# Kernel optimization log

Hardware: AMD Instinct MI355X
Metric: run time of the kernel (lower is better)

Reference implementation:

```python
import jax, jax.numpy as jnp
import numpy as np
import math

B, N, D = 16, 1024, 1024

def setup_inputs() -> dict:
    key = jax.random.key(0)
    k1, k2, k3, k4 = jax.random.split(key, 4)
    x = jax.random.normal(k1, (B, N, D), dtype=jnp.float32)
    # Keras 'random_normal' initializer defaults to stddev=0.05
    w_keys = jax.random.normal(k2, (N, N), dtype=jnp.float32) * 0.05
    w_queries = jax.random.normal(k3, (N, N), dtype=jnp.float32) * 0.05
    w_values = jax.random.normal(k4, (N, N), dtype=jnp.float32) * 0.05
    return {"x": x, "w_keys": w_keys, "w_queries": w_queries, "w_values": w_values}

def reference(x, w_keys, w_queries, w_values):
    # x: (B, N, D); weights: (N, N); fact = sqrt(N) per build(input_shape[1])
    fact = math.sqrt(x.shape[1])
    ip = jnp.swapaxes(x, 1, 2)              # (B, D, N)
    vk = ip @ w_keys                         # (B, D, N)
    vq = ip @ w_queries                      # (B, D, N)
    vv = ip @ w_values                       # (B, D, N)
    kq = jnp.einsum('bdn,ben->bde', vk, vq) / fact   # (B, D, D)
    sm = jax.nn.softmax(kq, axis=-1)         # softmax over last axis
    # tf: sm @ transpose(pm(vv)) == sm @ vv  since pm then transpose_b cancel
    out = jnp.einsum('bde,ben->bdn', sm, vv) # (B, D, N)
    return jnp.swapaxes(out, 1, 2)           # (B, N, D)
```

## Files before the change

### kernel.cpp

```cpp
#include <hip/hip_runtime.h>
#include <stdint.h>


typedef __bf16 bf16x8_t __attribute__((ext_vector_type(8)));
typedef float  f32x4_t  __attribute__((ext_vector_type(4)));

typedef __attribute__((address_space(3))) uint32_t as3_u32;
typedef __attribute__((address_space(1))) uint32_t as1_u32;

__device__ __forceinline__ void async_copy16(const void* g, const void* l) {
  __builtin_amdgcn_global_load_lds((const as1_u32*)(uintptr_t)g,
                                   (as3_u32*)(uint32_t)(uintptr_t)l,
                                   16, 0, 0);
}

__device__ __forceinline__ uint16_t f2bf(float f) {
  uint32_t x = __float_as_uint(f);
  return (uint16_t)((x + 0x7fffu + ((x >> 16) & 1u)) >> 16);
}
__device__ __forceinline__ float bf2f(uint16_t b) {
  return __uint_as_float(((uint32_t)b) << 16);
}

template <int EPI>
__device__ __forceinline__ void gemm_body(
    const uint16_t* __restrict__ A, const uint16_t* __restrict__ B,
    void* __restrict__ Cv, size_t sA, size_t sB, size_t sC,
    float alpha, float* __restrict__ Sp, int lid, char* smem)
{
  char* As = smem;
  char* Bs = smem + 32768;

  const int xcd  = lid & 7;
  const int slot = lid >> 3;
  const int z    = (xcd << 1) | (slot >> 5);
  const int t32  = slot & 31;
  const int bm0  = (t32 >> 3) << 8;
  const int bn0  = (t32 & 7) << 7;

  A += (size_t)z * sA + ((size_t)bm0 << 10);
  B += (size_t)z * sB + ((size_t)bn0 << 10);

  const int t    = threadIdx.x;
  const int lane = t & 63;
  const int w    = t >> 6;
  const int q    = lane >> 4;
  const int r16  = lane & 15;
  const int wm   = (w >> 1) << 6;
  const int wn   = (w & 1) << 6;

  const int g0  = t >> 3;
  const int cp  = t & 7;
  const int ce  = (cp ^ (g0 & 7)) << 3;
  const int so  = (g0 << 7) + (cp << 4);
  const uint16_t* Ag = A + ((size_t)g0 << 10) + ce;
  const uint16_t* Bg = B + ((size_t)g0 << 10) + ce;

  f32x4_t acc[4][4];
#pragma unroll
  for (int i = 0; i < 4; i++)
#pragma unroll
    for (int j = 0; j < 4; j++) acc[i][j] = (f32x4_t){0.f, 0.f, 0.f, 0.f};

  for (int k0 = 0; k0 < 1024; k0 += 64) {
#pragma unroll
    for (int s = 0; s < 4; ++s)
      async_copy16(Ag + (((size_t)s << 6) << 10) + k0, As + so + (s << 13));
#pragma unroll
    for (int s = 0; s < 2; ++s)
      async_copy16(Bg + (((size_t)s << 6) << 10) + k0, Bs + so + (s << 13));
    __syncthreads();

#pragma unroll
    for (int kk = 0; kk < 2; ++kk) {
      bf16x8_t af[4], bfr[4];
#pragma unroll
      for (int mi = 0; mi < 4; ++mi) {
        const int m = wm + (mi << 4) + r16;
        const int c = (kk << 2) + q;
        af[mi] = *(const bf16x8_t*)(As + (m << 7) + ((c ^ (m & 7)) << 4));
      }
#pragma unroll
      for (int ni = 0; ni < 4; ++ni) {
        const int n = wn + (ni << 4) + r16;
        const int c = (kk << 2) + q;
        bfr[ni] = *(const bf16x8_t*)(Bs + (n << 7) + ((c ^ (n & 7)) << 4));
      }
      __builtin_amdgcn_s_setprio(1);
#pragma unroll
      for (int mi = 0; mi < 4; ++mi)
#pragma unroll
        for (int ni = 0; ni < 4; ++ni)
          acc[mi][ni] = __builtin_amdgcn_mfma_f32_16x16x32_bf16(
              af[mi], bfr[ni], acc[mi][ni], 0, 0, 0);
      __builtin_amdgcn_s_setprio(0);
    }
    __syncthreads();
  }

  if constexpr (EPI == 3) {
    float inv[4];
#pragma unroll
    for (int ni = 0; ni < 4; ++ni) {
      const int c = bn0 + wn + (ni << 4) + r16;
      float S = 0.f;
#pragma unroll
      for (int p = 0; p < 16; ++p)
        S += Sp[((size_t)p << 14) + ((size_t)z << 10) + c];
      inv[ni] = 1.0f / S;
    }
    float* C = (float*)Cv + (size_t)z * sC;
#pragma unroll
    for (int mi = 0; mi < 4; ++mi)
#pragma unroll
      for (int ni = 0; ni < 4; ++ni)
#pragma unroll
        for (int r = 0; r < 4; ++r) {
          const int row = bm0 + wm + (mi << 4) + (q << 2) + r;
          const int col = bn0 + wn + (ni << 4) + r16;
          C[((size_t)row << 10) + col] = acc[mi][ni][r] * alpha * inv[ni];
        }
  } else {
    float* reg = (float*)smem + (size_t)w * 1056;
    uint16_t* C = (uint16_t*)Cv + (size_t)z * sC;
    float* SpW = Sp + ((size_t)(((bn0 >> 7) << 1) + (w & 1)) << 14)
                    + ((size_t)z << 10);
#pragma unroll
    for (int mi = 0; mi < 4; ++mi) {
      if constexpr (EPI == 2) {
        float ev[4][4];
#pragma unroll
        for (int ni = 0; ni < 4; ++ni)
#pragma unroll
          for (int r = 0; r < 4; ++r) {
            ev[ni][r] = __expf(acc[mi][ni][r] * alpha);
            reg[((q << 2) + r) * 66 + (ni << 4) + r16] = ev[ni][r];
          }
#pragma unroll
        for (int r = 0; r < 4; ++r) {
          float s = ev[0][r] + ev[1][r] + ev[2][r] + ev[3][r];
          s += __shfl_xor(s, 1, 16);
          s += __shfl_xor(s, 2, 16);
          s += __shfl_xor(s, 4, 16);
          s += __shfl_xor(s, 8, 16);
          if (r16 == 0)
            SpW[bm0 + wm + (mi << 4) + (q << 2) + r] = s;
        }
      } else {
#pragma unroll
        for (int ni = 0; ni < 4; ++ni)
#pragma unroll
          for (int r = 0; r < 4; ++r)
            reg[((q << 2) + r) * 66 + (ni << 4) + r16] = acc[mi][ni][r] * alpha;
      }
#pragma unroll
      for (int it = 0; it < 8; ++it) {
        const int rr = (it << 1) + (lane >> 5);
        const int cc = (lane & 31) << 1;
        const float2 v = *(const float2*)(reg + rr * 66 + cc);
        const uint32_t p = (uint32_t)f2bf(v.x) | ((uint32_t)f2bf(v.y) << 16);
        const int row = bm0 + wm + (mi << 4) + rr;
        const int col = bn0 + wn + cc;
        *(uint32_t*)(C + ((size_t)row << 10) + col) = p;
      }
    }
  }
}

template <int EPI>
__global__ __launch_bounds__(512, 4)
void gemm_bt256x128(const uint16_t* __restrict__ A,
                    const uint16_t* __restrict__ B,
                    void* __restrict__ Cv, size_t sA, size_t sB, size_t sC,
                    float alpha, float* __restrict__ Sp)
{
  __shared__ __align__(16) char smem[49152];
  gemm_body<EPI>(A, B, Cv, sA, sB, sC, alpha, Sp, blockIdx.x, smem);
}

__global__ __launch_bounds__(512, 4)
void gemm_pair(const uint16_t* __restrict__ A0, const uint16_t* __restrict__ B0,
               void* __restrict__ C0, size_t sA0, size_t sB0, size_t sC0,
               const uint16_t* __restrict__ A1, const uint16_t* __restrict__ B1,
               void* __restrict__ C1, size_t sA1, size_t sB1, size_t sC1)
{
  __shared__ __align__(16) char smem[49152];
  const int lid = blockIdx.x;
  if (lid < 512)
    gemm_body<0>(A0, B0, C0, sA0, sB0, sC0, 1.0f, nullptr, lid, smem);
  else
    gemm_body<0>(A1, B1, C1, sA1, sB1, sC1, 1.0f, nullptr, lid - 512, smem);
}

__global__ __launch_bounds__(256)
void transpose_splitk(const float* __restrict__ x, uint16_t* __restrict__ xT,
                      const uint16_t* __restrict__ Wqc,
                      const uint16_t* __restrict__ Wkc,
                      float* __restrict__ W2p)
{
  __shared__ __align__(16) char smem[32768];
  const int bx = blockIdx.x;
  const int t  = threadIdx.x;

  if (bx < 4096) {
    float (*tile)[65] = (float(*)[65])smem;
    const int z  = bx >> 8;
    const int r0 = ((bx >> 4) & 15) << 6;
    const int c0 = (bx & 15) << 6;
    const float* src = x + ((size_t)z << 20);
    uint16_t* dst = xT + ((size_t)z << 20);
    const int row  = t >> 4;
    const int col4 = (t & 15) << 2;
#pragma unroll
    for (int i = 0; i < 4; ++i) {
      const float4 v = *(const float4*)(
          src + (size_t)(r0 + row + (i << 4)) * 1024 + c0 + col4);
      float* tp = &tile[row + (i << 4)][col4];
      tp[0] = v.x; tp[1] = v.y; tp[2] = v.z; tp[3] = v.w;
    }
    __syncthreads();
#pragma unroll
    for (int p = 0; p < 2; ++p) {
      const int idx = (p << 8) + t;
      const int c  = idx >> 3;
      const int s8 = (idx & 7) << 3;
      uint32_t u0 = (uint32_t)f2bf(tile[s8 + 0][c]) |
                    ((uint32_t)f2bf(tile[s8 + 1][c]) << 16);
      uint32_t u1 = (uint32_t)f2bf(tile[s8 + 2][c]) |
                    ((uint32_t)f2bf(tile[s8 + 3][c]) << 16);
      uint32_t u2 = (uint32_t)f2bf(tile[s8 + 4][c]) |
                    ((uint32_t)f2bf(tile[s8 + 5][c]) << 16);
      uint32_t u3 = (uint32_t)f2bf(tile[s8 + 6][c]) |
                    ((uint32_t)f2bf(tile[s8 + 7][c]) << 16);
      uint4 pk; pk.x = u0; pk.y = u1; pk.z = u2; pk.w = u3;
      *(uint4*)(dst + (size_t)(c0 + c) * 1024 + r0 + s8) = pk;
    }
    return;
  }

  char* As = smem;
  char* Bs = smem + 16384;
  const int lid   = bx - 4096;
  const int slice = lid >> 6;
  const int tile4 = lid & 63;
  const int bm0   = (tile4 >> 3) << 7;
  const int bn0   = (tile4 & 7) << 7;
  const int koff  = slice << 8;

  const int lane = t & 63;
  const int w    = t >> 6;
  const int q    = lane >> 4;
  const int r16  = lane & 15;
  const int wm   = (w >> 1) << 6;
  const int wn   = (w & 1) << 6;

  f32x4_t acc[4][4];
#pragma unroll
  for (int i = 0; i < 4; i++)
#pragma unroll
    for (int j = 0; j < 4; j++) acc[i][j] = (f32x4_t){0.f, 0.f, 0.f, 0.f};

  for (int k0 = koff; k0 < koff + 256; k0 += 64) {
#pragma unroll
    for (int i = 0; i < 4; i++) {
      const int o  = (i << 12) + (t << 4);
      const int m  = o >> 7;
      const int cp = (o >> 4) & 7;
      const int c  = cp ^ (m & 7);
      async_copy16(Wqc + (size_t)(bm0 + m) * 1024 + (size_t)(k0 + (c << 3)),
                   As + o);
      async_copy16(Wkc + (size_t)(bn0 + m) * 1024 + (size_t)(k0 + (c << 3)),
                   Bs + o);
    }
    __syncthreads();
#pragma unroll
    for (int kk = 0; kk < 2; kk++) {
      bf16x8_t af[4], bfr[4];
#pragma unroll
      for (int mi = 0; mi < 4; mi++) {
        const int m = wm + (mi << 4) + r16;
        const int c = (kk << 2) + q;
        af[mi] = *(const bf16x8_t*)(As + (m << 7) + ((c ^ (m & 7)) << 4));
      }
#pragma unroll
      for (int ni = 0; ni < 4; ni++) {
        const int n = wn + (ni << 4) + r16;
        const int c = (kk << 2) + q;
        bfr[ni] = *(const bf16x8_t*)(Bs + (n << 7) + ((c ^ (n & 7)) << 4));
      }
#pragma unroll
      for (int mi = 0; mi < 4; mi++)
#pragma unroll
        for (int ni = 0; ni < 4; ni++)
          acc[mi][ni] = __builtin_amdgcn_mfma_f32_16x16x32_bf16(
              af[mi], bfr[ni], acc[mi][ni], 0, 0, 0);
    }
    __syncthreads();
  }

  float* C = W2p + (size_t)slice * (1024u * 1024u);
#pragma unroll
  for (int mi = 0; mi < 4; mi++)
#pragma unroll
    for (int ni = 0; ni < 4; ni++)
#pragma unroll
      for (int r = 0; r < 4; r++) {
        const int row = bm0 + wm + (mi << 4) + (q << 2) + r;
        const int col = bn0 + wn + (ni << 4) + r16;
        C[((size_t)row << 10) + col] = acc[mi][ni][r];
      }
}

__global__ __launch_bounds__(256)
void reduce_w2t(const float* __restrict__ P, uint16_t* __restrict__ W)
{
  const size_t i4 = (((size_t)blockIdx.x << 8) + threadIdx.x) << 2;
  const float4 a = *(const float4*)(P + i4);
  const float4 b = *(const float4*)(P + (1u << 20) + i4);
  const float4 c = *(const float4*)(P + (2u << 20) + i4);
  const float4 d = *(const float4*)(P + (3u << 20) + i4);
  ushort4 r;
  r.x = f2bf(a.x + b.x + c.x + d.x);
  r.y = f2bf(a.y + b.y + c.y + d.y);
  r.z = f2bf(a.z + b.z + c.z + d.z);
  r.w = f2bf(a.w + b.w + c.w + d.w);
  *(ushort4*)(W + i4) = r;
}

__global__ __launch_bounds__(256)
void prep_w(const float* __restrict__ w0, const float* __restrict__ w1,
            const float* __restrict__ w2, uint16_t* __restrict__ o0,
            uint16_t* __restrict__ o1, uint16_t* __restrict__ o2)
{
  __shared__ float tile[32][33];
  const int z = blockIdx.z;
  const int c0 = blockIdx.x << 5;
  const int r0 = blockIdx.y << 5;
  const int t = threadIdx.x;
  if (z < 2) {
    const float* src = z ? w1 : w0;
    uint16_t* dst = z ? o1 : o0;
    const int row = t >> 3;
    const int c4  = (t & 7) << 2;
    const float4 v =
        *(const float4*)(src + (size_t)(r0 + row) * 1024 + c0 + c4);
    ushort4 u;
    u.x = f2bf(v.x); u.y = f2bf(v.y); u.z = f2bf(v.z); u.w = f2bf(v.w);
    *(ushort4*)(dst + (size_t)(r0 + row) * 1024 + c0 + c4) = u;
  } else {
    const int tx = t & 31, ty = t >> 5;
#pragma unroll
    for (int i = 0; i < 32; i += 8)
      tile[ty + i][tx] = w2[(size_t)(r0 + ty + i) * 1024 + (c0 + tx)];
    __syncthreads();
#pragma unroll
    for (int i = 0; i < 32; i += 8)
      o2[(size_t)(c0 + ty + i) * 1024 + (r0 + tx)] = f2bf(tile[tx][ty + i]);
  }
}

extern "C" void kernel_launch(void* const* d_in, const int* in_sizes, int n_in,
                              void* d_out, int out_size, void* d_ws, size_t ws_size,
                              hipStream_t stream)
{
  const float* x  = (const float*)d_in[0];
  const float* wk = (const float*)d_in[1];
  const float* wq = (const float*)d_in[2];
  const float* wv = (const float*)d_in[3];
  float* out = (float*)d_out;

  constexpr int N = 1024;
  constexpr size_t DN = (size_t)N * N;

  char* ws = (char*)d_ws;
  uint16_t* xT   = (uint16_t*)(ws);
  uint16_t* Wkc  = (uint16_t*)(ws + (32ull << 20));
  uint16_t* Wqc  = (uint16_t*)(ws + (34ull << 20));
  uint16_t* Wtv  = (uint16_t*)(ws + (36ull << 20));
  uint16_t* W2Tc = (uint16_t*)(ws + (38ull << 20));
  float*    W2p  = (float*)   (ws + (40ull << 20));
  uint16_t* tmp  = (uint16_t*)(ws + (56ull << 20));
  uint16_t* vvT  = (uint16_t*)(ws + (88ull << 20));
  uint16_t* P    = (uint16_t*)(ws + (120ull << 20));
  float*    Spart= (float*)   (ws + (152ull << 20));

  prep_w<<<dim3(N / 32, N / 32, 3), 256, 0, stream>>>(wk, wq, wv, Wkc, Wqc, Wtv);
  transpose_splitk<<<4352, 256, 0, stream>>>(x, xT, Wqc, Wkc, W2p);
  reduce_w2t<<<1024, 256, 0, stream>>>(W2p, W2Tc);
  gemm_pair<<<1024, 512, 0, stream>>>(xT, W2Tc, tmp, DN, 0, DN,
                                      Wtv, xT, vvT, 0, DN, DN);
  gemm_bt256x128<2><<<512, 512, 0, stream>>>(tmp, xT, P, DN, DN, DN, 0.03125f, Spart);
  gemm_bt256x128<3><<<512, 512, 0, stream>>>(vvT, P, out, DN, DN, DN, 1.0f, Spart);
}
```

Baseline: 278.6 us.

## Fuse weight prep, Wq·Wkᵀ product and x transpose into one launch

Three launches (weight conversion, transpose plus split-K weight GEMM, partial-sum reduction) become one kernel. The Wq·Wkᵀ product is now computed by 64 blocks over the full K, converting fp32 to bf16 on the fly while staging into LDS. This removes the fp32 partial buffer, the reduction pass and two launch gaps. The tradeoff is that only 64 blocks each run a 1024-deep K loop with synchronous loads, which may lengthen the critical path while the other blocks do the transpose.

```diff
diff --git a/kernel.cpp b/kernel.cpp
--- a/kernel.cpp
+++ b/kernel.cpp
@@ -193,20 +193,102 @@
 }
 
 __global__ __launch_bounds__(256)
-void transpose_splitk(const float* __restrict__ x, uint16_t* __restrict__ xT,
-                      const uint16_t* __restrict__ Wqc,
-                      const uint16_t* __restrict__ Wkc,
-                      float* __restrict__ W2p)
+void prep_all(const float* __restrict__ x, uint16_t* __restrict__ xT,
+              const float* __restrict__ wq, const float* __restrict__ wk,
+              const float* __restrict__ wv, uint16_t* __restrict__ W2Tc,
+              uint16_t* __restrict__ Wtv)
 {
   __shared__ __align__(16) char smem[32768];
   const int bx = blockIdx.x;
   const int t  = threadIdx.x;
 
-  if (bx < 4096) {
+  if (bx < 64) {
+    char* As = smem;
+    char* Bs = smem + 16384;
+    const int bm0 = (bx >> 3) << 7;
+    const int bn0 = (bx & 7) << 7;
+    const int lane = t & 63;
+    const int w4 = t >> 6;
+    const int q = lane >> 4;
+    const int r16 = lane & 15;
+    const int wm = (w4 >> 1) << 6;
+    const int wn = (w4 & 1) << 6;
+    const int g0 = t >> 1;
+    const int kh = (t & 1) << 5;
+    const float* srcA = wq + (size_t)(bm0 + g0) * 1024 + kh;
+    const float* srcB = wk + (size_t)(bn0 + g0) * 1024 + kh;
+
+    f32x4_t acc[4][4];
+#pragma unroll
+    for (int i = 0; i < 4; i++)
+#pragma unroll
+      for (int j = 0; j < 4; j++) acc[i][j] = (f32x4_t){0.f, 0.f, 0.f, 0.f};
+
+    for (int k0 = 0; k0 < 1024; k0 += 64) {
+#pragma unroll
+      for (int j = 0; j < 4; ++j) {
+        const int c  = ((t & 1) << 2) + j;
+        const int cp = c ^ (g0 & 7);
+        const float4 a0 = *(const float4*)(srcA + k0 + (j << 3));
+        const float4 a1 = *(const float4*)(srcA + k0 + (j << 3) + 4);
+        const float4 b0 = *(const float4*)(srcB + k0 + (j << 3));
+        const float4 b1 = *(const float4*)(srcB + k0 + (j << 3) + 4);
+        uint4 pa, pb;
+        pa.x = (uint32_t)f2bf(a0.x) | ((uint32_t)f2bf(a0.y) << 16);
+        pa.y = (uint32_t)f2bf(a0.z) | ((uint32_t)f2bf(a0.w) << 16);
+        pa.z = (uint32_t)f2bf(a1.x) | ((uint32_t)f2bf(a1.y) << 16);
+        pa.w = (uint32_t)f2bf(a1.z) | ((uint32_t)f2bf(a1.w) << 16);
+        pb.x = (uint32_t)f2bf(b0.x) | ((uint32_t)f2bf(b0.y) << 16);
+        pb.y = (uint32_t)f2bf(b0.z) | ((uint32_t)f2bf(b0.w) << 16);
+        pb.z = (uint32_t)f2bf(b1.x) | ((uint32_t)f2bf(b1.y) << 16);
+        pb.w = (uint32_t)f2bf(b1.z) | ((uint32_t)f2bf(b1.w) << 16);
+        *(uint4*)(As + (g0 << 7) + (cp << 4)) = pa;
+        *(uint4*)(Bs + (g0 << 7) + (cp << 4)) = pb;
+      }
+      __syncthreads();
+#pragma unroll
+      for (int kk = 0; kk < 2; kk++) {
+        bf16x8_t af[4], bfr[4];
+#pragma unroll
+        for (int mi = 0; mi < 4; mi++) {
+          const int m = wm + (mi << 4) + r16;
+          const int c = (kk << 2) + q;
+          af[mi] = *(const bf16x8_t*)(As + (m << 7) + ((c ^ (m & 7)) << 4));
+        }
+#pragma unroll
+        for (int ni = 0; ni < 4; ni++) {
+          const int n = wn + (ni << 4) + r16;
+          const int c = (kk << 2) + q;
+          bfr[ni] = *(const bf16x8_t*)(Bs + (n << 7) + ((c ^ (n & 7)) << 4));
+        }
+#pragma unroll
+        for (int mi = 0; mi < 4; mi++)
+#pragma unroll
+          for (int ni = 0; ni < 4; ni++)
+            acc[mi][ni] = __builtin_amdgcn_mfma_f32_16x16x32_bf16(
+                af[mi], bfr[ni], acc[mi][ni], 0, 0, 0);
+      }
+      __syncthreads();
+    }
+#pragma unroll
+    for (int mi = 0; mi < 4; mi++)
+#pragma unroll
+      for (int ni = 0; ni < 4; ni++)
+#pragma unroll
+        for (int r = 0; r < 4; r++) {
+          const int row = bm0 + wm + (mi << 4) + (q << 2) + r;
+          const int col = bn0 + wn + (ni << 4) + r16;
+          W2Tc[((size_t)row << 10) + col] = f2bf(acc[mi][ni][r]);
+        }
+    return;
+  }
+
+  if (bx < 4160) {
     float (*tile)[65] = (float(*)[65])smem;
-    const int z  = bx >> 8;
-    const int r0 = ((bx >> 4) & 15) << 6;
-    const int c0 = (bx & 15) << 6;
+    const int bxx = bx - 64;
+    const int z  = bxx >> 8;
+    const int r0 = ((bxx >> 4) & 15) << 6;
+    const int c0 = (bxx & 15) << 6;
     const float* src = x + ((size_t)z << 20);
     uint16_t* dst = xT + ((size_t)z << 20);
     const int row  = t >> 4;
@@ -238,124 +320,19 @@
     return;
   }
 
-  char* As = smem;
-  char* Bs = smem + 16384;
-  const int lid   = bx - 4096;
-  const int slice = lid >> 6;
-  const int tile4 = lid & 63;
-  const int bm0   = (tile4 >> 3) << 7;
-  const int bn0   = (tile4 & 7) << 7;
-  const int koff  = slice << 8;
-
-  const int lane = t & 63;
-  const int w    = t >> 6;
-  const int q    = lane >> 4;
-  const int r16  = lane & 15;
-  const int wm   = (w >> 1) << 6;
-  const int wn   = (w & 1) << 6;
-
-  f32x4_t acc[4][4];
-#pragma unroll
-  for (int i = 0; i < 4; i++)
-#pragma unroll
-    for (int j = 0; j < 4; j++) acc[i][j] = (f32x4_t){0.f, 0.f, 0.f, 0.f};
-
-  for (int k0 = koff; k0 < koff + 256; k0 += 64) {
-#pragma unroll
-    for (int i = 0; i < 4; i++) {
-      const int o  = (i << 12) + (t << 4);
-      const int m  = o >> 7;
-      const int cp = (o >> 4) & 7;
-      const int c  = cp ^ (m & 7);
-      async_copy16(Wqc + (size_t)(bm0 + m) * 1024 + (size_t)(k0 + (c << 3)),
-                   As + o);
-      async_copy16(Wkc + (size_t)(bn0 + m) * 1024 + (size_t)(k0 + (c << 3)),
-                   Bs + o);
-    }
+  {
+    float (*tile)[33] = (float(*)[33])smem;
+    const int bxw = bx - 4160;
+    const int r0 = (bxw >> 5) << 5;
+    const int c0 = (bxw & 31) << 5;
+    const int tx = t & 31, ty = t >> 5;
+#pragma unroll
+    for (int i = 0; i < 32; i += 8)
+      tile[ty + i][tx] = wv[(size_t)(r0 + ty + i) * 1024 + (c0 + tx)];
     __syncthreads();
 #pragma unroll
-    for (int kk = 0; kk < 2; kk++) {
-      bf16x8_t af[4], bfr[4];
-#pragma unroll
-      for (int mi = 0; mi < 4; mi++) {
-        const int m = wm + (mi << 4) + r16;
-        const int c = (kk << 2) + q;
-        af[mi] = *(const bf16x8_t*)(As + (m << 7) + ((c ^ (m & 7)) << 4));
-      }
-#pragma unroll
-      for (int ni = 0; ni < 4; ni++) {
-        const int n = wn + (ni << 4) + r16;
-        const int c = (kk << 2) + q;
-        bfr[ni] = *(const bf16x8_t*)(Bs + (n << 7) + ((c ^ (n & 7)) << 4));
-      }
-#pragma unroll
-      for (int mi = 0; mi < 4; mi++)
-#pragma unroll
-        for (int ni = 0; ni < 4; ni++)
-          acc[mi][ni] = __builtin_amdgcn_mfma_f32_16x16x32_bf16(
-              af[mi], bfr[ni], acc[mi][ni], 0, 0, 0);
-    }
-    __syncthreads();
-  }
-
-  float* C = W2p + (size_t)slice * (1024u * 1024u);
-#pragma unroll
-  for (int mi = 0; mi < 4; mi++)
-#pragma unroll
-    for (int ni = 0; ni < 4; ni++)
-#pragma unroll
-      for (int r = 0; r < 4; r++) {
-        const int row = bm0 + wm + (mi << 4) + (q << 2) + r;
-        const int col = bn0 + wn + (ni << 4) + r16;
-        C[((size_t)row << 10) + col] = acc[mi][ni][r];
-      }
-}
-
-__global__ __launch_bounds__(256)
-void reduce_w2t(const float* __restrict__ P, uint16_t* __restrict__ W)
-{
-  const size_t i4 = (((size_t)blockIdx.x << 8) + threadIdx.x) << 2;
-  const float4 a = *(const float4*)(P + i4);
-  const float4 b = *(const float4*)(P + (1u << 20) + i4);
-  const float4 c = *(const float4*)(P + (2u << 20) + i4);
-  const float4 d = *(const float4*)(P + (3u << 20) + i4);
-  ushort4 r;
-  r.x = f2bf(a.x + b.x + c.x + d.x);
-  r.y = f2bf(a.y + b.y + c.y + d.y);
-  r.z = f2bf(a.z + b.z + c.z + d.z);
-  r.w = f2bf(a.w + b.w + c.w + d.w);
-  *(ushort4*)(W + i4) = r;
-}
-
-__global__ __launch_bounds__(256)
-void prep_w(const float* __restrict__ w0, const float* __restrict__ w1,
-            const float* __restrict__ w2, uint16_t* __restrict__ o0,
-            uint16_t* __restrict__ o1, uint16_t* __restrict__ o2)
-{
-  __shared__ float tile[32][33];
-  const int z = blockIdx.z;
-  const int c0 = blockIdx.x << 5;
-  const int r0 = blockIdx.y << 5;
-  const int t = threadIdx.x;
-  if (z < 2) {
-    const float* src = z ? w1 : w0;
-    uint16_t* dst = z ? o1 : o0;
-    const int row = t >> 3;
-    const int c4  = (t & 7) << 2;
-    const float4 v =
-        *(const float4*)(src + (size_t)(r0 + row) * 1024 + c0 + c4);
-    ushort4 u;
-    u.x = f2bf(v.x); u.y = f2bf(v.y); u.z = f2bf(v.z); u.w = f2bf(v.w);
-    *(ushort4*)(dst + (size_t)(r0 + row) * 1024 + c0 + c4) = u;
-  } else {
-    const int tx = t & 31, ty = t >> 5;
-#pragma unroll
     for (int i = 0; i < 32; i += 8)
-      tile[ty + i][tx] = w2[(size_t)(r0 + ty + i) * 1024 + (c0 + tx)];
-    __syncthreads();
-#pragma unroll
-    for (int i = 0; i < 32; i += 8)
-      o2[(size_t)(c0 + ty + i) * 1024 + (r0 + tx)] = f2bf(tile[tx][ty + i]);
+      Wtv[(size_t)(c0 + ty + i) * 1024 + (r0 + tx)] = f2bf(tile[tx][ty + i]);
   }
 }
 
@@ -374,19 +351,14 @@
 
   char* ws = (char*)d_ws;
   uint16_t* xT   = (uint16_t*)(ws);
-  uint16_t* Wkc  = (uint16_t*)(ws + (32ull << 20));
-  uint16_t* Wqc  = (uint16_t*)(ws + (34ull << 20));
   uint16_t* Wtv  = (uint16_t*)(ws + (36ull << 20));
   uint16_t* W2Tc = (uint16_t*)(ws + (38ull << 20));
-  float*    W2p  = (float*)   (ws + (40ull << 20));
   uint16_t* tmp  = (uint16_t*)(ws + (56ull << 20));
   uint16_t* vvT  = (uint16_t*)(ws + (88ull << 20));
   uint16_t* P    = (uint16_t*)(ws + (120ull << 20));
   float*    Spart= (float*)   (ws + (152ull << 20));
 
-  prep_w<<<dim3(N / 32, N / 32, 3), 256, 0, stream>>>(wk, wq, wv, Wkc, Wqc, Wtv);
-  transpose_splitk<<<4352, 256, 0, stream>>>(x, xT, Wqc, Wkc, W2p);
-  reduce_w2t<<<1024, 256, 0, stream>>>(W2p, W2Tc);
+  prep_all<<<5184, 256, 0, stream>>>(x, xT, wq, wk, wv, W2Tc, Wtv);
   gemm_pair<<<1024, 512, 0, stream>>>(xT, W2Tc, tmp, DN, 0, DN,
                                       Wtv, xT, vvT, 0, DN, DN);
   gemm_bt256x128<2><<<512, 512, 0, stream>>>(tmp, xT, P, DN, DN, DN, 0.03125f, Spart);
```

New measurement: 295.2 us. +5.9%, slower.
